# Kernel tuning notes

Hardware: AMD Instinct MI355X
Metric: run time of the kernel (lower is better)

The kernel has to match this reference:

```python
import jax, jax.numpy as jnp
import numpy as np

HID = 16

def setup_inputs() -> dict:
    key = jax.random.key(0)
    ks = jax.random.split(key, 10)
    B, T = 32768, 1024
    s_ih = 1.0 / np.sqrt(HID)
    def unif(k, shape):
        return jax.random.uniform(k, shape, jnp.float32, -s_ih, s_ih)
    return {
        "x": jax.random.normal(ks[0], (B, T, 1), jnp.float32),
        "W_ih": unif(ks[1], (4 * HID, 1)),       # torch LSTM weight_ih_l0, gate order i,f,g,o
        "W_hh": unif(ks[2], (4 * HID, HID)),     # weight_hh_l0
        "b_ih": unif(ks[3], (4 * HID,)),
        "b_hh": unif(ks[4], (4 * HID,)),
        "W1": unif(ks[5], (32, HID)),            # linear1 weight [out,in]
        "b1": unif(ks[6], (32,)),
        "W2": unif(ks[7], (6, 32)),              # linear2 weight
        "b2": unif(ks[8], (6,)),
    }

def _lstm_last_h(x, W_ih, W_hh, b_ih, b_hh):
    # x: [B, T, 1] -> scan over time
    B = x.shape[0]
    # Precompute input projections for all steps: [T, B, 4H]
    xg = jnp.einsum('bti,gi->tbg', x, W_ih) + (b_ih + b_hh)
    h0 = jnp.zeros((B, HID), x.dtype)
    c0 = jnp.zeros((B, HID), x.dtype)
    def step(carry, xg_t):
        h, c = carry
        gates = xg_t + h @ W_hh.T  # [B, 4H]
        i, f, g, o = jnp.split(gates, 4, axis=-1)
        i = jax.nn.sigmoid(i); f = jax.nn.sigmoid(f)
        g = jnp.tanh(g); o = jax.nn.sigmoid(o)
        c = f * c + i * g
        h = o * jnp.tanh(c)
        return (h, c), None
    (h_last, _), _ = jax.lax.scan(step, (h0, c0), xg)
    return h_last  # [B, H]

def reference(x, W_ih, W_hh, b_ih, b_hh, W1, b1, W2, b2):
    h = _lstm_last_h(x, W_ih, W_hh, b_ih, b_hh)          # [B, 16]
    h = jax.nn.relu(h @ W1.T + b1)                       # [B, 32]
    logits = h @ W2.T + b2                               # [B, 6]
    return jax.nn.log_softmax(logits, axis=1)
```

## Files before the change

### kernel.cpp

```cpp
#include <hip/hip_runtime.h>

#define TT 1024
#define LOG2E 1.4426950408889634f
#define LN2   0.6931471805599453f

typedef __attribute__((ext_vector_type(2))) float f32x2;
typedef __attribute__((ext_vector_type(4))) float f32x4;
typedef __attribute__((ext_vector_type(2))) _Float16 half2_t;
typedef __attribute__((ext_vector_type(4))) _Float16 half4;
typedef __attribute__((ext_vector_type(2))) __fp16 fp16x2_raw;

#if __has_builtin(__builtin_amdgcn_exp2f)
#define EXP2F(x) __builtin_amdgcn_exp2f(x)
#else
#define EXP2F(x) exp2f(x)
#endif
#if __has_builtin(__builtin_amdgcn_logf)
#define LOG2F(x) __builtin_amdgcn_logf(x)
#else
#define LOG2F(x) log2f(x)
#endif
#define RCPF(x) __builtin_amdgcn_rcpf(x)

__global__ __launch_bounds__(256, 2)
void lstm_head_kernel(const float* __restrict__ x,
                      const float* __restrict__ W_ih,
                      const float* __restrict__ W_hh,
                      const float* __restrict__ b_ih,
                      const float* __restrict__ b_hh,
                      const float* __restrict__ W1,
                      const float* __restrict__ b1,
                      const float* __restrict__ W2,
                      const float* __restrict__ b2,
                      float* __restrict__ out)
{
    __shared__ float lds_f[4][16 * 17];

    const int tid  = threadIdx.x;
    const int wib  = tid >> 6;
    const int lane = tid & 63;
    const int n    = lane & 15;
    const int q    = lane >> 4;
    const int batch0 = (blockIdx.x * 4 + wib) * 16;

    const float KG = 2.0f * LOG2E;

    half4 wfrag[4];
    f32x2 wih[4][2];
    f32x2 bias[4][2];
    #pragma unroll
    for (int g = 0; g < 4; ++g) {
        const float sc = (g == 2) ? KG : -LOG2E;
        const int arow = g * 16 + n;
        half4 wf;
        #pragma unroll
        for (int i = 0; i < 4; ++i)
            wf[i] = (_Float16)(W_hh[arow * 16 + (q * 4 + i)] * sc);
        wfrag[g] = wf;
        #pragma unroll
        for (int p = 0; p < 2; ++p) {
            const int row0 = g * 16 + q * 4 + 2 * p;
            wih[g][p]  = (f32x2){W_ih[row0] * sc, W_ih[row0 + 1] * sc};
            bias[g][p] = (f32x2){(b_ih[row0] + b_hh[row0]) * sc,
                                 (b_ih[row0 + 1] + b_hh[row0 + 1]) * sc};
        }
    }

    half4 hfrag = {(_Float16)0.f, (_Float16)0.f, (_Float16)0.f, (_Float16)0.f};
    f32x2 Cs[2] = {(f32x2){0.f, 0.f}, (f32x2){0.f, 0.f}};
    f32x2 hv[2] = {(f32x2){0.f, 0.f}, (f32x2){0.f, 0.f}};

    const float* xp = x + (size_t)(batch0 + n) * TT;

    for (int t4 = 0; t4 < TT; t4 += 4) {
        const float4 xv = *(const float4*)(xp + t4);
        const float xs4[4] = {xv.x, xv.y, xv.z, xv.w};

        #pragma unroll
        for (int s = 0; s < 4; ++s) {
            const float xs = xs4[s];
            f32x4 acc[4];
            #pragma unroll
            for (int g = 0; g < 4; ++g) {
                const f32x2 ci0 = __builtin_elementwise_fma(wih[g][0], (f32x2)xs, bias[g][0]);
                const f32x2 ci1 = __builtin_elementwise_fma(wih[g][1], (f32x2)xs, bias[g][1]);
                const f32x4 ci = {ci0.x, ci0.y, ci1.x, ci1.y};
                acc[g] = __builtin_amdgcn_mfma_f32_16x16x16f16(wfrag[g], hfrag, ci, 0, 0, 0);
            }

            half2_t hh[2];
            #pragma unroll
            for (int p = 0; p < 2; ++p) {
                const f32x2 ai = {acc[0][2*p], acc[0][2*p + 1]};
                const f32x2 af = {acc[1][2*p], acc[1][2*p + 1]};
                const f32x2 ag = {acc[2][2*p], acc[2][2*p + 1]};
                const f32x2 ao = {acc[3][2*p], acc[3][2*p + 1]};

                const f32x2 ei = {EXP2F(ai.x), EXP2F(ai.y)};
                const f32x2 ef = {EXP2F(af.x), EXP2F(af.y)};
                const f32x2 eg = {EXP2F(ag.x), EXP2F(ag.y)};
                const f32x2 eo = {EXP2F(ao.x), EXP2F(ao.y)};

                const f32x2 pei = ei + 1.0f;
                const f32x2 pef = ef + 1.0f;
                const f32x2 egp = eg + 1.0f;
                const f32x2 egm = __builtin_elementwise_fma((f32x2)KG, eg, (f32x2)(-KG));
                const f32x2 P   = pei * egp;
                const f32x2 D   = pef * P;
                const f32x2 t2  = pef * egm;
                const f32x2 num = __builtin_elementwise_fma(Cs[p], P, t2);
                const f32x2 rD  = {RCPF(D.x), RCPF(D.y)};
                const f32x2 Cn  = num * rD;
                Cs[p] = Cn;

                const f32x2 ec  = {EXP2F(Cn.x), EXP2F(Cn.y)};
                const f32x2 peo = eo + 1.0f;
                const f32x2 ecp = ec + 1.0f;
                const f32x2 ecm = ec - 1.0f;
                const f32x2 D2  = peo * ecp;
                const f32x2 rD2 = {RCPF(D2.x), RCPF(D2.y)};
                const f32x2 h2  = ecm * rD2;
                hv[p] = h2;
                hh[p] = __builtin_bit_cast(half2_t, __builtin_amdgcn_cvt_pkrtz(h2.x, h2.y));
            }
            hfrag = (half4){hh[0].x, hh[0].y, hh[1].x, hh[1].y};
        }
    }

    float* fh = lds_f[wib];
    #pragma unroll
    for (int p = 0; p < 2; ++p) {
        fh[n * 17 + (q * 4 + 2*p)]     = hv[p].x;
        fh[n * 17 + (q * 4 + 2*p + 1)] = hv[p].y;
    }

    if (lane < 16) {
        const int b = batch0 + lane;
        float hvv[16];
        #pragma unroll
        for (int j = 0; j < 16; ++j) hvv[j] = fh[lane * 17 + j];

        float a1[32];
        #pragma unroll
        for (int u = 0; u < 32; ++u) {
            float s = b1[u];
            #pragma unroll
            for (int j = 0; j < 16; ++j) s = fmaf(W1[u * 16 + j], hvv[j], s);
            a1[u] = fmaxf(s, 0.0f);
        }

        float z[6];
        float m = -1e30f;
        #pragma unroll
        for (int v = 0; v < 6; ++v) {
            float s = b2[v];
            #pragma unroll
            for (int u = 0; u < 32; ++u) s = fmaf(W2[v * 32 + u], a1[u], s);
            z[v] = s;
            m = fmaxf(m, s);
        }
        float se = 0.0f;
        #pragma unroll
        for (int v = 0; v < 6; ++v) se += EXP2F((z[v] - m) * LOG2E);
        const float lse = m + LOG2F(se) * LN2;
        #pragma unroll
        for (int v = 0; v < 6; ++v) out[b * 6 + v] = z[v] - lse;
    }
}

extern "C" void kernel_launch(void* const* d_in, const int* in_sizes, int n_in,
                              void* d_out, int out_size, void* d_ws, size_t ws_size,
                              hipStream_t stream) {
    const float* x    = (const float*)d_in[0];
    const float* W_ih = (const float*)d_in[1];
    const float* W_hh = (const float*)d_in[2];
    const float* b_ih = (const float*)d_in[3];
    const float* b_hh = (const float*)d_in[4];
    const float* W1   = (const float*)d_in[5];
    const float* b1   = (const float*)d_in[6];
    const float* W2   = (const float*)d_in[7];
    const float* b2   = (const float*)d_in[8];
    float* out = (float*)d_out;

    const int B = out_size / 6;
    const int nblocks = B / 64;

    hipLaunchKernelGGL(lstm_head_kernel, dim3(nblocks), dim3(256), 0, stream,
                       x, W_ih, W_hh, b_ih, b_hh, W1, b1, W2, b2, out);
}
```

Measured before the change: 592.6 us.

## Interleave two independent batch tiles per wavefront and prefetch next inputs

Each wavefront now carries two independent 16-batch LSTM recurrences (A and B) and interleaves their MFMA and activation chains. This hides the serial dependency latency of the per-step recurrence. It also prefetches the next four timesteps of x one iteration ahead. Grid size is halved and the launch-bounds occupancy hint drops from 2 to 1, which raises register pressure and reduces the wave count across the GPU.

```diff
diff --git a/kernel.cpp b/kernel.cpp
--- a/kernel.cpp
+++ b/kernel.cpp
@@ -8,7 +8,6 @@
 typedef __attribute__((ext_vector_type(4))) float f32x4;
 typedef __attribute__((ext_vector_type(2))) _Float16 half2_t;
 typedef __attribute__((ext_vector_type(4))) _Float16 half4;
-typedef __attribute__((ext_vector_type(2))) __fp16 fp16x2_raw;
 
 #if __has_builtin(__builtin_amdgcn_exp2f)
 #define EXP2F(x) __builtin_amdgcn_exp2f(x)
@@ -22,7 +21,7 @@
 #endif
 #define RCPF(x) __builtin_amdgcn_rcpf(x)
 
-__global__ __launch_bounds__(256, 2)
+__global__ __launch_bounds__(256, 1)
 void lstm_head_kernel(const float* __restrict__ x,
                       const float* __restrict__ W_ih,
                       const float* __restrict__ W_hh,
@@ -34,14 +33,14 @@
                       const float* __restrict__ b2,
                       float* __restrict__ out)
 {
-    __shared__ float lds_f[4][16 * 17];
+    __shared__ float lds_f[4][32 * 17];
 
     const int tid  = threadIdx.x;
     const int wib  = tid >> 6;
     const int lane = tid & 63;
     const int n    = lane & 15;
     const int q    = lane >> 4;
-    const int batch0 = (blockIdx.x * 4 + wib) * 16;
+    const int batch0 = (blockIdx.x * 4 + wib) * 32;
 
     const float KG = 2.0f * LOG2E;
 
@@ -66,75 +65,135 @@
         }
     }
 
-    half4 hfrag = {(_Float16)0.f, (_Float16)0.f, (_Float16)0.f, (_Float16)0.f};
-    f32x2 Cs[2] = {(f32x2){0.f, 0.f}, (f32x2){0.f, 0.f}};
-    f32x2 hv[2] = {(f32x2){0.f, 0.f}, (f32x2){0.f, 0.f}};
-
-    const float* xp = x + (size_t)(batch0 + n) * TT;
+    half4 hfragA = {(_Float16)0.f, (_Float16)0.f, (_Float16)0.f, (_Float16)0.f};
+    half4 hfragB = hfragA;
+    f32x2 CsA[2] = {(f32x2){0.f, 0.f}, (f32x2){0.f, 0.f}};
+    f32x2 CsB[2] = {(f32x2){0.f, 0.f}, (f32x2){0.f, 0.f}};
+    f32x2 hvA[2] = {(f32x2){0.f, 0.f}, (f32x2){0.f, 0.f}};
+    f32x2 hvB[2] = {(f32x2){0.f, 0.f}, (f32x2){0.f, 0.f}};
+
+    const float* xpA = x + (size_t)(batch0 + n) * TT;
+    const float* xpB = x + (size_t)(batch0 + 16 + n) * TT;
+
+    float4 xvA = *(const float4*)(xpA);
+    float4 xvB = *(const float4*)(xpB);
 
     for (int t4 = 0; t4 < TT; t4 += 4) {
-        const float4 xv = *(const float4*)(xp + t4);
-        const float xs4[4] = {xv.x, xv.y, xv.z, xv.w};
+        const int tnext = (t4 + 4) & (TT - 1);
+        const float4 prefA = *(const float4*)(xpA + tnext);
+        const float4 prefB = *(const float4*)(xpB + tnext);
+
+        const float xsA4[4] = {xvA.x, xvA.y, xvA.z, xvA.w};
+        const float xsB4[4] = {xvB.x, xvB.y, xvB.z, xvB.w};
 
         #pragma unroll
         for (int s = 0; s < 4; ++s) {
-            const float xs = xs4[s];
-            f32x4 acc[4];
+            const float xsA = xsA4[s];
+            const float xsB = xsB4[s];
+            f32x4 accA[4], accB[4];
             #pragma unroll
             for (int g = 0; g < 4; ++g) {
-                const f32x2 ci0 = __builtin_elementwise_fma(wih[g][0], (f32x2)xs, bias[g][0]);
-                const f32x2 ci1 = __builtin_elementwise_fma(wih[g][1], (f32x2)xs, bias[g][1]);
-                const f32x4 ci = {ci0.x, ci0.y, ci1.x, ci1.y};
-                acc[g] = __builtin_amdgcn_mfma_f32_16x16x16f16(wfrag[g], hfrag, ci, 0, 0, 0);
+                const f32x2 cA0 = __builtin_elementwise_fma(wih[g][0], (f32x2)xsA, bias[g][0]);
+                const f32x2 cA1 = __builtin_elementwise_fma(wih[g][1], (f32x2)xsA, bias[g][1]);
+                const f32x4 cA = {cA0.x, cA0.y, cA1.x, cA1.y};
+                accA[g] = __builtin_amdgcn_mfma_f32_16x16x16f16(wfrag[g], hfragA, cA, 0, 0, 0);
             }
-
-            half2_t hh[2];
+            #pragma unroll
+            for (int g = 0; g < 4; ++g) {
+                const f32x2 cB0 = __builtin_elementwise_fma(wih[g][0], (f32x2)xsB, bias[g][0]);
+                const f32x2 cB1 = __builtin_elementwise_fma(wih[g][1], (f32x2)xsB, bias[g][1]);
+                const f32x4 cB = {cB0.x, cB0.y, cB1.x, cB1.y};
+                accB[g] = __builtin_amdgcn_mfma_f32_16x16x16f16(wfrag[g], hfragB, cB, 0, 0, 0);
+            }
+
+            half2_t hhA[2], hhB[2];
             #pragma unroll
             for (int p = 0; p < 2; ++p) {
-                const f32x2 ai = {acc[0][2*p], acc[0][2*p + 1]};
-                const f32x2 af = {acc[1][2*p], acc[1][2*p + 1]};
-                const f32x2 ag = {acc[2][2*p], acc[2][2*p + 1]};
-                const f32x2 ao = {acc[3][2*p], acc[3][2*p + 1]};
-
-                const f32x2 ei = {EXP2F(ai.x), EXP2F(ai.y)};
-                const f32x2 ef = {EXP2F(af.x), EXP2F(af.y)};
-                const f32x2 eg = {EXP2F(ag.x), EXP2F(ag.y)};
-                const f32x2 eo = {EXP2F(ao.x), EXP2F(ao.y)};
-
-                const f32x2 pei = ei + 1.0f;
-                const f32x2 pef = ef + 1.0f;
-                const f32x2 egp = eg + 1.0f;
-                const f32x2 egm = __builtin_elementwise_fma((f32x2)KG, eg, (f32x2)(-KG));
-                const f32x2 P   = pei * egp;
-                const f32x2 D   = pef * P;
-                const f32x2 t2  = pef * egm;
-                const f32x2 num = __builtin_elementwise_fma(Cs[p], P, t2);
-                const f32x2 rD  = {RCPF(D.x), RCPF(D.y)};
-                const f32x2 Cn  = num * rD;
-                Cs[p] = Cn;
-
-                const f32x2 ec  = {EXP2F(Cn.x), EXP2F(Cn.y)};
-                const f32x2 peo = eo + 1.0f;
-                const f32x2 ecp = ec + 1.0f;
-                const f32x2 ecm = ec - 1.0f;
-                const f32x2 D2  = peo * ecp;
-                const f32x2 rD2 = {RCPF(D2.x), RCPF(D2.y)};
-                const f32x2 h2  = ecm * rD2;
-                hv[p] = h2;
-                hh[p] = __builtin_bit_cast(half2_t, __builtin_amdgcn_cvt_pkrtz(h2.x, h2.y));
+                {
+                    const f32x2 ai = {accA[0][2*p], accA[0][2*p + 1]};
+                    const f32x2 af = {accA[1][2*p], accA[1][2*p + 1]};
+                    const f32x2 ag = {accA[2][2*p], accA[2][2*p + 1]};
+                    const f32x2 ao = {accA[3][2*p], accA[3][2*p + 1]};
+
+                    const f32x2 ei = {EXP2F(ai.x), EXP2F(ai.y)};
+                    const f32x2 ef = {EXP2F(af.x), EXP2F(af.y)};
+                    const f32x2 eg = {EXP2F(ag.x), EXP2F(ag.y)};
+                    const f32x2 eo = {EXP2F(ao.x), EXP2F(ao.y)};
+
+                    const f32x2 pei = ei + 1.0f;
+                    const f32x2 pef = ef + 1.0f;
+                    const f32x2 egp = eg + 1.0f;
+                    const f32x2 egm = __builtin_elementwise_fma((f32x2)KG, eg, (f32x2)(-KG));
+                    const f32x2 P   = pei * egp;
+                    const f32x2 D   = pef * P;
+                    const f32x2 t2  = pef * egm;
+                    const f32x2 num = __builtin_elementwise_fma(CsA[p], P, t2);
+                    const f32x2 rD  = {RCPF(D.x), RCPF(D.y)};
+                    const f32x2 Cn  = num * rD;
+                    CsA[p] = Cn;
+
+                    const f32x2 ec  = {EXP2F(Cn.x), EXP2F(Cn.y)};
+                    const f32x2 peo = eo + 1.0f;
+                    const f32x2 ecp = ec + 1.0f;
+                    const f32x2 ecm = ec - 1.0f;
+                    const f32x2 D2  = peo * ecp;
+                    const f32x2 rD2 = {RCPF(D2.x), RCPF(D2.y)};
+                    const f32x2 h2  = ecm * rD2;
+                    hvA[p] = h2;
+                    hhA[p] = __builtin_bit_cast(half2_t, __builtin_amdgcn_cvt_pkrtz(h2.x, h2.y));
+                }
+                {
+                    const f32x2 ai = {accB[0][2*p], accB[0][2*p + 1]};
+                    const f32x2 af = {accB[1][2*p], accB[1][2*p + 1]};
+                    const f32x2 ag = {accB[2][2*p], accB[2][2*p + 1]};
+                    const f32x2 ao = {accB[3][2*p], accB[3][2*p + 1]};
+
+                    const f32x2 ei = {EXP2F(ai.x), EXP2F(ai.y)};
+                    const f32x2 ef = {EXP2F(af.x), EXP2F(af.y)};
+                    const f32x2 eg = {EXP2F(ag.x), EXP2F(ag.y)};
+                    const f32x2 eo = {EXP2F(ao.x), EXP2F(ao.y)};
+
+                    const f32x2 pei = ei + 1.0f;
+                    const f32x2 pef = ef + 1.0f;
+                    const f32x2 egp = eg + 1.0f;
+                    const f32x2 egm = __builtin_elementwise_fma((f32x2)KG, eg, (f32x2)(-KG));
+                    const f32x2 P   = pei * egp;
+                    const f32x2 D   = pef * P;
+                    const f32x2 t2  = pef * egm;
+                    const f32x2 num = __builtin_elementwise_fma(CsB[p], P, t2);
+                    const f32x2 rD  = {RCPF(D.x), RCPF(D.y)};
+                    const f32x2 Cn  = num * rD;
+                    CsB[p] = Cn;
+
+                    const f32x2 ec  = {EXP2F(Cn.x), EXP2F(Cn.y)};
+                    const f32x2 peo = eo + 1.0f;
+                    const f32x2 ecp = ec + 1.0f;
+                    const f32x2 ecm = ec - 1.0f;
+                    const f32x2 D2  = peo * ecp;
+                    const f32x2 rD2 = {RCPF(D2.x), RCPF(D2.y)};
+                    const f32x2 h2  = ecm * rD2;
+                    hvB[p] = h2;
+                    hhB[p] = __builtin_bit_cast(half2_t, __builtin_amdgcn_cvt_pkrtz(h2.x, h2.y));
+                }
             }
-            hfrag = (half4){hh[0].x, hh[0].y, hh[1].x, hh[1].y};
-        }
+            hfragA = (half4){hhA[0].x, hhA[0].y, hhA[1].x, hhA[1].y};
+            hfragB = (half4){hhB[0].x, hhB[0].y, hhB[1].x, hhB[1].y};
+        }
+
+        xvA = prefA;
+        xvB = prefB;
     }
 
     float* fh = lds_f[wib];
     #pragma unroll
     for (int p = 0; p < 2; ++p) {
-        fh[n * 17 + (q * 4 + 2*p)]     = hv[p].x;
-        fh[n * 17 + (q * 4 + 2*p + 1)] = hv[p].y;
-    }
-
-    if (lane < 16) {
+        fh[n * 17 + (q * 4 + 2*p)]            = hvA[p].x;
+        fh[n * 17 + (q * 4 + 2*p + 1)]        = hvA[p].y;
+        fh[(16 + n) * 17 + (q * 4 + 2*p)]     = hvB[p].x;
+        fh[(16 + n) * 17 + (q * 4 + 2*p + 1)] = hvB[p].y;
+    }
+
+    if (lane < 32) {
         const int b = batch0 + lane;
         float hvv[16];
         #pragma unroll
@@ -183,7 +242,7 @@
     float* out = (float*)d_out;
 
     const int B = out_size / 6;
-    const int nblocks = B / 64;
+    const int nblocks = B / 128;
 
     hipLaunchKernelGGL(lstm_head_kernel, dim3(nblocks), dim3(256), 0, stream,
                        x, W_ih, W_hh, b_ih, b_hh, W1, b1, W2, b2, out);
```

New measurement: 801.8 us. 35.3% more time.
